# Kernel optimization log

Measured on AMD Instinct MI355X. Metric: run time of the kernel, lower is better.

Reference implementation:

```python
import jax, jax.numpy as jnp
import numpy as np

D_MODEL = 1024
N_HEADS = 16
D_K = D_MODEL // N_HEADS
D_FF = 4096
EPS = 1e-5


def _layernorm(x, g, b):
    mu = jnp.mean(x, axis=-1, keepdims=True)
    var = jnp.mean(jnp.square(x - mu), axis=-1, keepdims=True)
    return (x - mu) * jax.lax.rsqrt(var + EPS) * g + b


def setup_inputs() -> dict:
    key = jax.random.key(0)
    ks = jax.random.split(key, 16)
    s = 0.02
    B, S = 2, 2048
    inp = {
        "x": jax.random.normal(ks[0], (B, S, D_MODEL), dtype=jnp.float32),
        "mask": jnp.ones((1, 1, S, S), dtype=jnp.int32),
        # attention projections (stored [in, out]; y = x @ W + b)
        "Wq": jax.random.normal(ks[1], (D_MODEL, D_MODEL)) * s,
        "bq": jnp.zeros((D_MODEL,)),
        "Wk": jax.random.normal(ks[2], (D_MODEL, D_MODEL)) * s,
        "bk": jnp.zeros((D_MODEL,)),
        "Wv": jax.random.normal(ks[3], (D_MODEL, D_MODEL)) * s,
        "bv": jnp.zeros((D_MODEL,)),
        "Wo": jax.random.normal(ks[4], (D_MODEL, D_MODEL)) * s,
        "bo": jnp.zeros((D_MODEL,)),
        "temperature": jnp.sqrt(jnp.array([float(D_K)], dtype=jnp.float32)),
        "time_weights": jax.random.normal(ks[5], (1, N_HEADS, 1, D_K)),
        "gateW": jax.random.normal(ks[6], (D_K, 1)) * s,
        "gateb": jnp.zeros((1,)),
        "ln_attn_g": jnp.ones((D_MODEL,)),
        "ln_attn_b": jnp.zeros((D_MODEL,)),
        # feed-forward
        "fc1W": jax.random.normal(ks[7], (D_MODEL, D_FF)) * s,
        "fc1b": jnp.zeros((D_FF,)),
        "fc2W": jax.random.normal(ks[8], (D_FF, D_MODEL)) * s,
        "fc2b": jnp.zeros((D_MODEL,)),
        "n1g": jnp.ones((D_MODEL,)),
        "n1b": jnp.zeros((D_MODEL,)),
        "n2g": jnp.ones((D_MODEL,)),
        "n2b": jnp.zeros((D_MODEL,)),
    }
    return inp


def reference(x, mask, Wq, bq, Wk, bk, Wv, bv, Wo, bo, temperature,
              time_weights, gateW, gateb, ln_attn_g, ln_attn_b,
              fc1W, fc1b, fc2W, fc2b, n1g, n1b, n2g, n2b):
    B, S, D = x.shape
    H, dk = N_HEADS, D_K

    def heads(t):  # [B,S,D] -> [B,H,S,dk]
        return t.reshape(B, S, H, dk).transpose(0, 2, 1, 3)

    q = heads(x @ Wq + bq) + time_weights  # learned per-head bias on Q
    k = heads(x @ Wk + bk)
    v = heads(x @ Wv + bv)

    scores = jnp.einsum("bhqd,bhkd->bhqk", q, k) / temperature
    scores = jnp.where(mask == 0, jnp.float32(-1e9), scores)
    gate = jax.nn.sigmoid(q @ gateW + gateb)  # [B,H,S,1] per-query gate
    scores = scores * gate
    probs = jax.nn.softmax(scores, axis=-1)

    ctx = jnp.einsum("bhqk,bhkd->bhqd", probs, v)
    ctx = ctx.transpose(0, 2, 1, 3).reshape(B, S, D)
    attn_out = _layernorm(ctx @ Wo + bo, ln_attn_g, ln_attn_b)

    x1 = _layernorm(x + attn_out, n1g, n1b)
    ff = jax.nn.gelu(x1 @ fc1W + fc1b, approximate=False) @ fc2W + fc2b
    return _layernorm(x1 + ff, n2g, n2b)
```

## Files before the change

### kernel.cpp

```cpp
#include <hip/hip_runtime.h>
#include <stdint.h>
#include <math.h>


typedef uint16_t u16;
typedef unsigned long long u64;
typedef __attribute__((ext_vector_type(8))) short short8;
typedef __attribute__((ext_vector_type(4))) float f32x4;

#define S_LEN 2048
#define DM 1024
#define PSTR 76

#define GLOAD_LDS16(g, l)                                                      \
  __builtin_amdgcn_global_load_lds(                                            \
      (const __attribute__((address_space(1))) void*)(g),                      \
      (__attribute__((address_space(3))) void*)(l), 16, 0, 0)

#define VM0_BARRIER()                                                          \
  do {                                                                         \
    asm volatile("s_waitcnt vmcnt(0)" ::: "memory");                           \
    __builtin_amdgcn_s_barrier();                                              \
  } while (0)

#define LGKM_BARRIER()                                                         \
  do {                                                                         \
    asm volatile("s_waitcnt lgkmcnt(0)" ::: "memory");                         \
    __builtin_amdgcn_s_barrier();                                              \
  } while (0)

__device__ __forceinline__ float bf2f(u16 h) {
  union { uint32_t u; float f; } x;
  x.u = ((uint32_t)h) << 16;
  return x.f;
}
__device__ __forceinline__ u16 f2bf(float f) {
  union { float f; uint32_t u; } x;
  x.f = f;
  uint32_t r = (x.u + 0x7fffu + ((x.u >> 16) & 1u)) >> 16;
  return (u16)r;
}
__device__ __forceinline__ u16 f2bf_fast(float f) {
  union { float f; uint32_t u; } x;
  x.f = f;
  return (u16)((x.u + 0x8000u) >> 16);
}

__device__ __forceinline__ float gelu_ex(float v) {
  float x = fabsf(v) * 0.70710678118654752f;
  float t = __builtin_amdgcn_rcpf(__builtin_fmaf(0.3275911f, x, 1.0f));
  float p = 1.061405429f;
  p = __builtin_fmaf(p, t, -1.453152027f);
  p = __builtin_fmaf(p, t, 1.421413741f);
  p = __builtin_fmaf(p, t, -0.284496736f);
  p = __builtin_fmaf(p, t, 0.254829592f);
  p = p * t;
  float ex = __builtin_amdgcn_exp2f(-1.4426950408889634f * x * x);
  float er = __builtin_fmaf(-p, ex, 1.0f);
  er = (v < 0.f) ? -er : er;
  return 0.5f * v * (1.0f + er);
}

union U8 { uint4 u; u16 s[8]; };
union U4 { uint2 u; u16 s[4]; };

__global__ __launch_bounds__(256) void cvt_k(const float* __restrict__ in,
                                             u16* __restrict__ out, int n) {
  int i = (blockIdx.x * 256 + threadIdx.x) * 4;
  if (i >= n) return;
  float4 v = *(const float4*)(in + i);
  U4 o;
  o.s[0] = f2bf(v.x); o.s[1] = f2bf(v.y); o.s[2] = f2bf(v.z); o.s[3] = f2bf(v.w);
  *(uint2*)(out + i) = o.u;
}

__global__ __launch_bounds__(256) void mb_k(const int* __restrict__ mask,
                                            u16* __restrict__ mb) {
  int tid = blockIdx.x * 256 + threadIdx.x;
  const int* src = mask + (size_t)tid * 16;
  uint32_t b = 0;
#pragma unroll
  for (int q = 0; q < 4; q++) {
    int4 m = *(const int4*)(src + q * 4);
    b |= (m.x != 0 ? 1u : 0u) << (q * 4 + 0);
    b |= (m.y != 0 ? 1u : 0u) << (q * 4 + 1);
    b |= (m.z != 0 ? 1u : 0u) << (q * 4 + 2);
    b |= (m.w != 0 ? 1u : 0u) << (q * 4 + 3);
  }
  mb[tid] = (u16)b;
}

__device__ __forceinline__ void tcvt_body(const float* __restrict__ in,
                                          u16* __restrict__ out, int R, int C) {
  __shared__ u16 tile[64][72];
  int c0 = blockIdx.x * 64, r0 = blockIdx.y * 64;
  int t = threadIdx.x;
  int r = t & 63, seg = t >> 6;
  const float* src = in + (size_t)(r0 + r) * C + c0 + seg * 16;
#pragma unroll
  for (int q = 0; q < 4; q++) {
    float4 v = *(const float4*)(src + q * 4);
    tile[r][seg * 16 + q * 4 + 0] = f2bf(v.x);
    tile[r][seg * 16 + q * 4 + 1] = f2bf(v.y);
    tile[r][seg * 16 + q * 4 + 2] = f2bf(v.z);
    tile[r][seg * 16 + q * 4 + 3] = f2bf(v.w);
  }
  __syncthreads();
  U8 v0, v1;
#pragma unroll
  for (int i = 0; i < 8; i++) v0.s[i] = tile[seg * 16 + i][r];
#pragma unroll
  for (int i = 0; i < 8; i++) v1.s[i] = tile[seg * 16 + 8 + i][r];
  u16* dst = out + (size_t)(c0 + r) * R + r0 + seg * 16;
  *(uint4*)dst = v0.u;
  *(uint4*)(dst + 8) = v1.u;
}

__global__ __launch_bounds__(256) void transpose_cvt_k(const float* __restrict__ in,
                                                       u16* __restrict__ out,
                                                       int R, int C) {
  tcvt_body(in, out, R, C);
}

__global__ __launch_bounds__(256) void transpose_cvt3_k(const float* __restrict__ i0,
                                                        const float* __restrict__ i1,
                                                        const float* __restrict__ i2,
                                                        u16* __restrict__ o0,
                                                        u16* __restrict__ o1,
                                                        u16* __restrict__ o2) {
  int z = blockIdx.z;
  const float* in = (z == 0) ? i0 : (z == 1) ? i1 : i2;
  u16* out = (z == 0) ? o0 : (z == 1) ? o1 : o2;
  tcvt_body(in, out, 1024, 1024);
}

__global__ __launch_bounds__(256) void vtrans_k(const u16* __restrict__ V,
                                                u16* __restrict__ VT) {
  __shared__ u16 tile[64][72];
  int bx = blockIdx.x, bh = blockIdx.y;
  int b = bh >> 4, h = bh & 15;
  int t = threadIdx.x, r = t & 63, seg = t >> 6;
  const u16* src = V + (size_t)(b * S_LEN + bx * 64 + r) * DM + h * 64 + seg * 16;
  *(uint4*)&tile[r][seg * 16] = *(const uint4*)src;
  *(uint4*)&tile[r][seg * 16 + 8] = *(const uint4*)(src + 8);
  __syncthreads();
  U8 v0, v1;
#pragma unroll
  for (int i = 0; i < 8; i++) v0.s[i] = tile[seg * 16 + i][r];
#pragma unroll
  for (int i = 0; i < 8; i++) v1.s[i] = tile[seg * 16 + 8 + i][r];
  u16* dst = VT + ((size_t)bh * 64 + r) * S_LEN + bx * 64 + seg * 16;
  *(uint4*)dst = v0.u;
  *(uint4*)(dst + 8) = v1.u;
}

template <int BM, int EPI, int MXS>
__global__ __launch_bounds__(256) void gemm_bt(const u16* __restrict__ A,
                                               const u16* __restrict__ Bt,
                                               u16* __restrict__ C,
                                               const float* __restrict__ bias,
                                               int M, int N, int K) {
  constexpr int MI = BM / 32;
  constexpr int RPW = BM / 4;
  __shared__ u16 As[2][BM * 32];
  __shared__ u16 Bs[2][128 * 32];
  int t = threadIdx.x;
  int wid = t >> 6, lane = t & 63;
  int g = lane >> 4, li = lane & 15;
  int bx = MXS ? blockIdx.y : blockIdx.x;
  int by = MXS ? blockIdx.x : blockIdx.y;
  int wr = (wid >> 1) * (BM / 2), wc = (wid & 1) * 64;

  const u16* a0 = A + (size_t)(by * BM + wid * RPW + (lane >> 2)) * K + (lane & 3) * 8;
  const u16* b0 = Bt + (size_t)(bx * 128 + wid * 32 + (lane >> 2)) * K + (lane & 3) * 8;
  u16* lA[2] = {&As[0][wid * RPW * 32], &As[1][wid * RPW * 32]};
  u16* lB[2] = {&Bs[0][wid * 1024], &Bs[1][wid * 1024]};

  f32x4 acc[MI][4];
#pragma unroll
  for (int i = 0; i < MI; i++)
#pragma unroll
    for (int j = 0; j < 4; j++) acc[i][j] = (f32x4){0.f, 0.f, 0.f, 0.f};

  auto stage = [&](int buf, int kk) {
    GLOAD_LDS16(a0 + kk, lA[buf]);
    if (BM == 128) GLOAD_LDS16(a0 + (size_t)16 * K + kk, lA[buf] + 512);
    GLOAD_LDS16(b0 + kk, lB[buf]);
    GLOAD_LDS16(b0 + (size_t)16 * K + kk, lB[buf] + 512);
  };
  auto compute = [&](int buf) {
    short8 af[MI], bfv[4];
#pragma unroll
    for (int i = 0; i < MI; i++)
      af[i] = *(const short8*)&As[buf][(wr + i * 16 + li) * 32 + g * 8];
#pragma unroll
    for (int i = 0; i < 4; i++)
      bfv[i] = *(const short8*)&Bs[buf][(wc + i * 16 + li) * 32 + g * 8];
    __builtin_amdgcn_s_setprio(1);
#pragma unroll
    for (int mi = 0; mi < MI; mi++)
#pragma unroll
      for (int ni = 0; ni < 4; ni++)
        acc[mi][ni] = __builtin_amdgcn_mfma_f32_16x16x32_bf16(
            af[mi], bfv[ni], acc[mi][ni], 0, 0, 0);
    __builtin_amdgcn_s_setprio(0);
  };

  stage(0, 0);
  VM0_BARRIER();
  for (int k0 = 0; k0 < K; k0 += 64) {
    stage(1, k0 + 32);
    compute(0);
    VM0_BARRIER();
    if (k0 + 64 < K) stage(0, k0 + 64);
    compute(1);
    VM0_BARRIER();
  }

#pragma unroll
  for (int ni = 0; ni < 4; ni++) {
    int col = bx * 128 + wc + ni * 16 + li;
    float bv = bias[col];
#pragma unroll
    for (int mi = 0; mi < MI; mi++) {
#pragma unroll
      for (int r = 0; r < 4; r++) {
        int row = by * BM + wr + mi * 16 + g * 4 + r;
        float v = acc[mi][ni][r] + bv;
        if (EPI == 2) v = gelu_ex(v);
        C[(size_t)row * N + col] = f2bf(v);
      }
    }
  }
}

__global__ __launch_bounds__(256) void qkv_gemm(const u16* __restrict__ A,
                                                const u16* __restrict__ WTq,
                                                const u16* __restrict__ WTk,
                                                const u16* __restrict__ WTv,
                                                u16* __restrict__ Cq,
                                                u16* __restrict__ Ck,
                                                u16* __restrict__ Cv,
                                                const float* __restrict__ bq,
                                                const float* __restrict__ bk,
                                                const float* __restrict__ bv,
                                                const float* __restrict__ tw) {
  const int K = 1024, N = 1024;
  __shared__ u16 As[2][128 * 32];
  __shared__ u16 Bs[2][128 * 32];
  int t = threadIdx.x;
  int wid = t >> 6, lane = t & 63;
  int g = lane >> 4, li = lane & 15;
  int by = blockIdx.x, bx = blockIdx.y, z = blockIdx.z;
  int wr = (wid >> 1) * 64, wc = (wid & 1) * 64;

  const u16* Bt = (z == 0) ? WTq : (z == 1) ? WTk : WTv;
  u16* C = (z == 0) ? Cq : (z == 1) ? Ck : Cv;
  const float* bias = (z == 0) ? bq : (z == 1) ? bk : bv;

  const u16* a0 = A + (size_t)(by * 128 + wid * 32 + (lane >> 2)) * K + (lane & 3) * 8;
  const u16* b0 = Bt + (size_t)(bx * 128 + wid * 32 + (lane >> 2)) * K + (lane & 3) * 8;
  u16* lA[2] = {&As[0][wid * 1024], &As[1][wid * 1024]};
  u16* lB[2] = {&Bs[0][wid * 1024], &Bs[1][wid * 1024]};

  f32x4 acc[4][4];
#pragma unroll
  for (int i = 0; i < 4; i++)
#pragma unroll
    for (int j = 0; j < 4; j++) acc[i][j] = (f32x4){0.f, 0.f, 0.f, 0.f};

  auto stage = [&](int buf, int kk) {
    GLOAD_LDS16(a0 + kk, lA[buf]);
    GLOAD_LDS16(a0 + (size_t)16 * K + kk, lA[buf] + 512);
    GLOAD_LDS16(b0 + kk, lB[buf]);
    GLOAD_LDS16(b0 + (size_t)16 * K + kk, lB[buf] + 512);
  };
  auto compute = [&](int buf) {
    short8 af[4], bfv[4];
#pragma unroll
    for (int i = 0; i < 4; i++)
      af[i] = *(const short8*)&As[buf][(wr + i * 16 + li) * 32 + g * 8];
#pragma unroll
    for (int i = 0; i < 4; i++)
      bfv[i] = *(const short8*)&Bs[buf][(wc + i * 16 + li) * 32 + g * 8];
    __builtin_amdgcn_s_setprio(1);
#pragma unroll
    for (int mi = 0; mi < 4; mi++)
#pragma unroll
      for (int ni = 0; ni < 4; ni++)
        acc[mi][ni] = __builtin_amdgcn_mfma_f32_16x16x32_bf16(
            af[mi], bfv[ni], acc[mi][ni], 0, 0, 0);
    __builtin_amdgcn_s_setprio(0);
  };

  stage(0, 0);
  VM0_BARRIER();
  for (int k0 = 0; k0 < K; k0 += 64) {
    stage(1, k0 + 32);
    compute(0);
    VM0_BARRIER();
    if (k0 + 64 < K) stage(0, k0 + 64);
    compute(1);
    VM0_BARRIER();
  }

#pragma unroll
  for (int ni = 0; ni < 4; ni++) {
    int col = bx * 128 + wc + ni * 16 + li;
    float bvv = bias[col];
    if (z == 0) bvv += tw[col];
#pragma unroll
    for (int mi = 0; mi < 4; mi++) {
#pragma unroll
      for (int r = 0; r < 4; r++) {
        int row = by * 128 + wr + mi * 16 + g * 4 + r;
        C[(size_t)row * N + col] = f2bf(acc[mi][ni][r] + bvv);
      }
    }
  }
}

__global__ __launch_bounds__(256) void attn_k(const u16* __restrict__ Q,
                                              const u16* __restrict__ Kp,
                                              const u16* __restrict__ VT,
                                              u16* __restrict__ CTX,
                                              const u16* __restrict__ mb,
                                              const float* __restrict__ gateW,
                                              const float* __restrict__ gateb,
                                              const float* __restrict__ temp) {
  __shared__ u16 QPs[64 * PSTR];
  __shared__ u16 Ks[64][72];
  __shared__ u16 Vs[64][72];
  __shared__ float gate_s[64];

  int blk = blockIdx.x;
  int bh = blk & 31, qt = blk >> 5;
  int b = bh >> 4, h = bh & 15;
  int t = threadIdx.x, wid = t >> 6, lane = t & 63;
  int g = lane >> 4, li = lane & 15;
  int sq0 = qt * 64;
  int rr = t >> 2, cc = (t & 3) * 16;

  const u16* Qb  = Q + ((size_t)b * S_LEN) * DM + h * 64;
  const u16* Kb  = Kp + ((size_t)b * S_LEN) * DM + h * 64;
  const u16* VTb = VT + ((size_t)(b * 16 + h) * 64) * S_LEN;

  {
    const u16* src = Qb + (size_t)(sq0 + rr) * DM + cc;
    *(uint4*)&QPs[rr * PSTR + cc] = *(const uint4*)src;
    *(uint4*)&QPs[rr * PSTR + cc + 8] = *(const uint4*)(src + 8);
  }
  __syncthreads();
  {
    U8 q0, q1;
    q0.u = *(const uint4*)&QPs[rr * PSTR + cc];
    q1.u = *(const uint4*)&QPs[rr * PSTR + cc + 8];
    float4 w0 = *(const float4*)(gateW + cc);
    float4 w1 = *(const float4*)(gateW + cc + 4);
    float4 w2 = *(const float4*)(gateW + cc + 8);
    float4 w3 = *(const float4*)(gateW + cc + 12);
    float acc;
    acc  = bf2f(q0.s[0]) * w0.x + bf2f(q0.s[1]) * w0.y +
           bf2f(q0.s[2]) * w0.z + bf2f(q0.s[3]) * w0.w;
    acc += bf2f(q0.s[4]) * w1.x + bf2f(q0.s[5]) * w1.y +
           bf2f(q0.s[6]) * w1.z + bf2f(q0.s[7]) * w1.w;
    acc += bf2f(q1.s[0]) * w2.x + bf2f(q1.s[1]) * w2.y +
           bf2f(q1.s[2]) * w2.z + bf2f(q1.s[3]) * w2.w;
    acc += bf2f(q1.s[4]) * w3.x + bf2f(q1.s[5]) * w3.y +
           bf2f(q1.s[6]) * w3.z + bf2f(q1.s[7]) * w3.w;
    acc += __shfl_xor(acc, 1, 64);
    acc += __shfl_xor(acc, 2, 64);
    if ((t & 3) == 0) gate_s[rr] = 1.f / (1.f + __expf(-(acc + gateb[0])));
  }
  __syncthreads();

  const float LOG2E = 1.4426950408889634f;
  float invt2 = LOG2E / temp[0];
  float cng = -1.0e9f * temp[0];
  short8 qf0 = *(const short8*)&QPs[(wid * 16 + li) * PSTR + g * 8];
  short8 qf1 = *(const short8*)&QPs[(wid * 16 + li) * PSTR + 32 + g * 8];
  float gqs[4];
  int row0 = sq0 + wid * 16 + g * 4;
#pragma unroll
  for (int r = 0; r < 4; r++) gqs[r] = gate_s[wid * 16 + g * 4 + r] * invt2;
  const u16* mbp = mb + (size_t)row0 * 128;

  float m_i[4], psl[4];
  f32x4 o[4];
#pragma unroll
  for (int r = 0; r < 4; r++) { m_i[r] = -1e30f; psl[r] = 0.f; }
#pragma unroll
  for (int n = 0; n < 4; n++) o[n] = (f32x4){0.f, 0.f, 0.f, 0.f};

  uint4 kxa, kxb, vxa, vxb;
  {
    const u16* sK = Kb + (size_t)rr * DM + cc;
    kxa = *(const uint4*)sK; kxb = *(const uint4*)(sK + 8);
    const u16* sV = VTb + (size_t)rr * S_LEN + cc;
    vxa = *(const uint4*)sV; vxb = *(const uint4*)(sV + 8);
  }

  for (int kt = 0; kt < 32; kt++) {
    LGKM_BARRIER();
    *(uint4*)&Ks[rr][cc]     = kxa;
    *(uint4*)&Ks[rr][cc + 8] = kxb;
    *(uint4*)&Vs[rr][cc]     = vxa;
    *(uint4*)&Vs[rr][cc + 8] = vxb;
    u64 bits[4];
#pragma unroll
    for (int r = 0; r < 4; r++)
      bits[r] = *(const u64*)(mbp + (size_t)r * 128 + kt * 4);
    if (kt + 1 < 32) {
      const u16* sK = Kb + (size_t)((kt + 1) * 64 + rr) * DM + cc;
      kxa = *(const uint4*)sK; kxb = *(const uint4*)(sK + 8);
      const u16* sV = VTb + (size_t)rr * S_LEN + (kt + 1) * 64 + cc;
      vxa = *(const uint4*)sV; vxb = *(const uint4*)(sV + 8);
    }
    LGKM_BARRIER();

    f32x4 sc[4];
#pragma unroll
    for (int ni = 0; ni < 4; ni++) {
      sc[ni] = (f32x4){0.f, 0.f, 0.f, 0.f};
      short8 kf0 = *(const short8*)&Ks[ni * 16 + li][g * 8];
      short8 kf1 = *(const short8*)&Ks[ni * 16 + li][32 + g * 8];
      sc[ni] = __builtin_amdgcn_mfma_f32_16x16x32_bf16(qf0, kf0, sc[ni], 0, 0, 0);
      sc[ni] = __builtin_amdgcn_mfma_f32_16x16x32_bf16(qf1, kf1, sc[ni], 0, 0, 0);
    }

    float rmax[4] = {-1e30f, -1e30f, -1e30f, -1e30f};
    bool allm = ((bits[0] & bits[1] & bits[2] & bits[3]) == ~0ull);
    if (__all(allm)) {
#pragma unroll
      for (int ni = 0; ni < 4; ni++)
#pragma unroll
        for (int r = 0; r < 4; r++) {
          float s = sc[ni][r] * gqs[r];
          sc[ni][r] = s;
          rmax[r] = fmaxf(rmax[r], s);
        }
    } else {
      u64 bs[4];
#pragma unroll
      for (int r = 0; r < 4; r++) bs[r] = bits[r] >> li;
#pragma unroll
      for (int ni = 0; ni < 4; ni++)
#pragma unroll
        for (int r = 0; r < 4; r++) {
          float s = ((bs[r] >> (ni * 16)) & 1ull) ? sc[ni][r] * gqs[r]
                                                  : gqs[r] * cng;
          sc[ni][r] = s;
          rmax[r] = fmaxf(rmax[r], s);
        }
    }
#pragma unroll
    for (int off = 1; off < 16; off <<= 1)
#pragma unroll
      for (int r = 0; r < 4; r++)
        rmax[r] = fmaxf(rmax[r], __shfl_xor(rmax[r], off, 64));

    bool need = false;
#pragma unroll
    for (int r = 0; r < 4; r++) need = need || (rmax[r] > m_i[r] + 8.f);
    if (__any(need)) {
#pragma unroll
      for (int r = 0; r < 4; r++) {
        float mnew = fmaxf(m_i[r], rmax[r]);
        float alpha = __builtin_amdgcn_exp2f(m_i[r] - mnew);
        m_i[r] = mnew;
        psl[r] *= alpha;
#pragma unroll
        for (int n = 0; n < 4; n++) o[n][r] *= alpha;
      }
    }

    float pp[4] = {0.f, 0.f, 0.f, 0.f};
#pragma unroll
    for (int ni = 0; ni < 4; ni++)
#pragma unroll
      for (int r = 0; r < 4; r++) {
        float p = __builtin_amdgcn_exp2f(sc[ni][r] - m_i[r]);
        pp[r] += p;
        QPs[(wid * 16 + g * 4 + r) * PSTR + ni * 16 + li] = f2bf_fast(p);
      }
#pragma unroll
    for (int r = 0; r < 4; r++) psl[r] += pp[r];

    __builtin_amdgcn_wave_barrier();

    short8 pf0 = *(const short8*)&QPs[(wid * 16 + li) * PSTR + g * 8];
    short8 pf1 = *(const short8*)&QPs[(wid * 16 + li) * PSTR + 32 + g * 8];
#pragma unroll
    for (int ni = 0; ni < 4; ni++) {
      short8 vf0 = *(const short8*)&Vs[ni * 16 + li][g * 8];
      short8 vf1 = *(const short8*)&Vs[ni * 16 + li][32 + g * 8];
      o[ni] = __builtin_amdgcn_mfma_f32_16x16x32_bf16(pf0, vf0, o[ni], 0, 0, 0);
      o[ni] = __builtin_amdgcn_mfma_f32_16x16x32_bf16(pf1, vf1, o[ni], 0, 0, 0);
    }
  }

  float linv[4];
#pragma unroll
  for (int r = 0; r < 4; r++) {
    float l = psl[r];
#pragma unroll
    for (int off = 1; off < 16; off <<= 1) l += __shfl_xor(l, off, 64);
    linv[r] = 1.f / l;
  }
#pragma unroll
  for (int ni = 0; ni < 4; ni++) {
    int col = h * 64 + ni * 16 + li;
#pragma unroll
    for (int r = 0; r < 4; r++) {
      size_t row = (size_t)b * S_LEN + row0 + r;
      CTX[row * DM + col] = f2bf(o[ni][r] * linv[r]);
    }
  }
}

__device__ __forceinline__ void block_sum2(float& a, float& b, float* red, int t) {
#pragma unroll
  for (int off = 32; off > 0; off >>= 1) {
    a += __shfl_xor(a, off, 64);
    b += __shfl_xor(b, off, 64);
  }
  __syncthreads();
  if ((t & 63) == 0) {
    red[(t >> 6) * 2] = a;
    red[(t >> 6) * 2 + 1] = b;
  }
  __syncthreads();
  a = red[0] + red[2] + red[4] + red[6];
  b = red[1] + red[3] + red[5] + red[7];
}

__global__ __launch_bounds__(256) void ln1_k(const u16* __restrict__ po,
                                             const float* __restrict__ x,
                                             const float* __restrict__ g1,
                                             const float* __restrict__ b1,
                                             const float* __restrict__ g2,
                                             const float* __restrict__ b2,
                                             u16* __restrict__ x1) {
  __shared__ float red[8];
  int row = blockIdx.x, t = threadIdx.x;
  size_t base = (size_t)row * 1024 + t * 4;
  U4 pv; pv.u = *(const uint2*)(po + base);
  float v[4];
#pragma unroll
  for (int i = 0; i < 4; i++) v[i] = bf2f(pv.s[i]);
  float s1 = v[0] + v[1] + v[2] + v[3];
  float s2 = v[0]*v[0] + v[1]*v[1] + v[2]*v[2] + v[3]*v[3];
  block_sum2(s1, s2, red, t);
  float mu = s1 * (1.f / 1024.f);
  float rs = rsqrtf(s2 * (1.f / 1024.f) - mu * mu + 1e-5f);
  float4 xv = *(const float4*)(x + base);
  float4 g1v = *(const float4*)(g1 + t * 4);
  float4 b1v = *(const float4*)(b1 + t * 4);
  float w[4];
  w[0] = xv.x + ((v[0] - mu) * rs * g1v.x + b1v.x);
  w[1] = xv.y + ((v[1] - mu) * rs * g1v.y + b1v.y);
  w[2] = xv.z + ((v[2] - mu) * rs * g1v.z + b1v.z);
  w[3] = xv.w + ((v[3] - mu) * rs * g1v.w + b1v.w);
  s1 = w[0] + w[1] + w[2] + w[3];
  s2 = w[0]*w[0] + w[1]*w[1] + w[2]*w[2] + w[3]*w[3];
  block_sum2(s1, s2, red, t);
  mu = s1 * (1.f / 1024.f);
  rs = rsqrtf(s2 * (1.f / 1024.f) - mu * mu + 1e-5f);
  float4 g2v = *(const float4*)(g2 + t * 4);
  float4 b2v = *(const float4*)(b2 + t * 4);
  U4 ov;
  ov.s[0] = f2bf((w[0] - mu) * rs * g2v.x + b2v.x);
  ov.s[1] = f2bf((w[1] - mu) * rs * g2v.y + b2v.y);
  ov.s[2] = f2bf((w[2] - mu) * rs * g2v.z + b2v.z);
  ov.s[3] = f2bf((w[3] - mu) * rs * g2v.w + b2v.w);
  *(uint2*)(x1 + base) = ov.u;
}

__global__ __launch_bounds__(256) void ln2_k(const u16* __restrict__ y,
                                             const u16* __restrict__ x1,
                                             const float* __restrict__ g,
                                             const float* __restrict__ b,
                                             float* __restrict__ out) {
  __shared__ float red[8];
  int row = blockIdx.x, t = threadIdx.x;
  size_t base = (size_t)row * 1024 + t * 4;
  U4 yv; yv.u = *(const uint2*)(y + base);
  U4 xv; xv.u = *(const uint2*)(x1 + base);
  float w[4];
#pragma unroll
  for (int i = 0; i < 4; i++) w[i] = bf2f(yv.s[i]) + bf2f(xv.s[i]);
  float s1 = w[0] + w[1] + w[2] + w[3];
  float s2 = w[0]*w[0] + w[1]*w[1] + w[2]*w[2] + w[3]*w[3];
  block_sum2(s1, s2, red, t);
  float mu = s1 * (1.f / 1024.f);
  float rs = rsqrtf(s2 * (1.f / 1024.f) - mu * mu + 1e-5f);
  float4 gv = *(const float4*)(g + t * 4);
  float4 bv = *(const float4*)(b + t * 4);
  float4 ov;
  ov.x = (w[0] - mu) * rs * gv.x + bv.x;
  ov.y = (w[1] - mu) * rs * gv.y + bv.y;
  ov.z = (w[2] - mu) * rs * gv.z + bv.z;
  ov.w = (w[3] - mu) * rs * gv.w + bv.w;
  *(float4*)(out + base) = ov;
}

extern "C" void kernel_launch(void* const* d_in, const int* in_sizes, int n_in,
                              void* d_out, int out_size, void* d_ws, size_t ws_size,
                              hipStream_t stream) {
  (void)in_sizes; (void)n_in; (void)out_size;
  const float* x    = (const float*)d_in[0];
  const int*   mask = (const int*)d_in[1];
  const float* Wq = (const float*)d_in[2];  const float* bq = (const float*)d_in[3];
  const float* Wk = (const float*)d_in[4];  const float* bk = (const float*)d_in[5];
  const float* Wv = (const float*)d_in[6];  const float* bv = (const float*)d_in[7];
  const float* Wo = (const float*)d_in[8];  const float* bo = (const float*)d_in[9];
  const float* temp = (const float*)d_in[10];
  const float* tw   = (const float*)d_in[11];
  const float* gW   = (const float*)d_in[12]; const float* gb  = (const float*)d_in[13];
  const float* lag  = (const float*)d_in[14]; const float* lab = (const float*)d_in[15];
  const float* f1W  = (const float*)d_in[16]; const float* f1b = (const float*)d_in[17];
  const float* f2W  = (const float*)d_in[18]; const float* f2b = (const float*)d_in[19];
  const float* n1g  = (const float*)d_in[20]; const float* n1b = (const float*)d_in[21];
  const float* n2g  = (const float*)d_in[22]; const float* n2b = (const float*)d_in[23];
  float* out = (float*)d_out;

  u16* ws = (u16*)d_ws;
  const size_t MB4 = (size_t)4096 * 1024;
  u16* s0 = ws;
  u16* s1 = ws + 1 * MB4;
  u16* s2 = ws + 2 * MB4;
  u16* s3 = ws + 3 * MB4;
  u16* s4 = ws + 4 * MB4;
  u16* d0 = (u16*)d_out;
  u16* d1 = d0 + MB4;
  bool bigws = ws_size >= (size_t)9 * 8 * 1024 * 1024;
  u16* Hfull = ws + 5 * MB4;

  dim3 blk(256);
  cvt_k<<<dim3(4096), blk, 0, stream>>>(x, s4, 4096 * 1024);
  transpose_cvt3_k<<<dim3(16, 16, 3), blk, 0, stream>>>(Wq, Wk, Wv, s0, s1, s2);
  qkv_gemm<<<dim3(32, 8, 3), blk, 0, stream>>>(s4, s0, s1, s2, s3, d0, d1,
                                               bq, bk, bv, tw);
  vtrans_k<<<dim3(32, 32), blk, 0, stream>>>(d1, s0);
  mb_k<<<dim3(1024), blk, 0, stream>>>(mask, s1);
  transpose_cvt_k<<<dim3(16, 16), blk, 0, stream>>>(Wo, s4, 1024, 1024);
  attn_k<<<dim3(1024), blk, 0, stream>>>(s3, d0, s0, s2, s1, gW, gb, temp);
  gemm_bt<64, 0, 1><<<dim3(64, 8), blk, 0, stream>>>(s2, s4, d0, bo, 4096, 1024, 1024);
  ln1_k<<<dim3(4096), blk, 0, stream>>>(d0, x, lag, lab, n1g, n1b, s3);
  transpose_cvt_k<<<dim3(64, 16), blk, 0, stream>>>(f1W, s0, 1024, 4096);
  transpose_cvt_k<<<dim3(16, 64), blk, 0, stream>>>(f2W, s1, 4096, 1024);
  if (bigws) {
    gemm_bt<128, 2, 0><<<dim3(32, 32), blk, 0, stream>>>(s3, s0, Hfull, f1b,
                                                         4096, 4096, 1024);
    gemm_bt<64, 0, 0><<<dim3(8, 64), blk, 0, stream>>>(Hfull, s1, s2, f2b,
                                                       4096, 1024, 4096);
  } else {
    for (int i = 0; i < 2; i++) {
      const u16* Ai = s3 + (size_t)i * 2048 * 1024;
      u16* Yi = s2 + (size_t)i * 2048 * 1024;
      gemm_bt<128, 2, 0><<<dim3(32, 16), blk, 0, stream>>>(Ai, s0, d0, f1b,
                                                           2048, 4096, 1024);
      gemm_bt<64, 0, 1><<<dim3(32, 8), blk, 0, stream>>>(d0, s1, Yi, f2b,
                                                         2048, 1024, 4096);
    }
  }
  ln2_k<<<dim3(4096), blk, 0, stream>>>(s2, s3, n2g, n2b, out);
}
```

Before: 468.0 us.

## Split attention key tiles across two wave groups and merge softmax partials

The attention kernel now launches 512 threads per block. Eight waves split each 64-key tile into two halves, so each wave handles 16 query rows against 32 keys. At the end the two halves' running max, sum and output accumulators are merged through shared memory using rescaling factors. This adds intra-block parallelism and shortens each wave's per-tile critical path, at the cost of a final merge step, extra shared memory and more threads per block.

New measurement: 485.1 us. 3.7% more time.

```diff
diff --git a/kernel.cpp b/kernel.cpp
--- a/kernel.cpp
+++ b/kernel.cpp
@@ -4,6 +4,7 @@
 
 
 typedef uint16_t u16;
+typedef uint32_t u32;
 typedef unsigned long long u64;
 typedef __attribute__((ext_vector_type(8))) short short8;
 typedef __attribute__((ext_vector_type(4))) float f32x4;
@@ -320,7 +321,7 @@
   }
 }
 
-__global__ __launch_bounds__(256) void attn_k(const u16* __restrict__ Q,
+__global__ __launch_bounds__(512) void attn_k(const u16* __restrict__ Q,
                                               const u16* __restrict__ Kp,
                                               const u16* __restrict__ VT,
                                               u16* __restrict__ CTX,
@@ -328,61 +329,54 @@
                                               const float* __restrict__ gateW,
                                               const float* __restrict__ gateb,
                                               const float* __restrict__ temp) {
-  __shared__ u16 QPs[64 * PSTR];
-  __shared__ u16 Ks[64][72];
-  __shared__ u16 Vs[64][72];
+  __shared__ u16 QPs[128 * PSTR];
+  __shared__ u16 KV[2 * 64 * 72];
   __shared__ float gate_s[64];
+  __shared__ float mps[4][16][2];
+
+  u16* Ks = KV;
+  u16* Vs = KV + 64 * 72;
 
   int blk = blockIdx.x;
   int bh = blk & 31, qt = blk >> 5;
   int b = bh >> 4, h = bh & 15;
   int t = threadIdx.x, wid = t >> 6, lane = t & 63;
   int g = lane >> 4, li = lane & 15;
+  int rg = wid & 3, kh = wid >> 2;
   int sq0 = qt * 64;
-  int rr = t >> 2, cc = (t & 3) * 16;
+  int rr = t >> 3, cs = (t & 7) * 8;
 
   const u16* Qb  = Q + ((size_t)b * S_LEN) * DM + h * 64;
   const u16* Kb  = Kp + ((size_t)b * S_LEN) * DM + h * 64;
   const u16* VTb = VT + ((size_t)(b * 16 + h) * 64) * S_LEN;
 
   {
-    const u16* src = Qb + (size_t)(sq0 + rr) * DM + cc;
-    *(uint4*)&QPs[rr * PSTR + cc] = *(const uint4*)src;
-    *(uint4*)&QPs[rr * PSTR + cc + 8] = *(const uint4*)(src + 8);
+    const u16* src = Qb + (size_t)(sq0 + rr) * DM + cs;
+    *(uint4*)&QPs[rr * PSTR + cs] = *(const uint4*)src;
   }
   __syncthreads();
   {
-    U8 q0, q1;
-    q0.u = *(const uint4*)&QPs[rr * PSTR + cc];
-    q1.u = *(const uint4*)&QPs[rr * PSTR + cc + 8];
-    float4 w0 = *(const float4*)(gateW + cc);
-    float4 w1 = *(const float4*)(gateW + cc + 4);
-    float4 w2 = *(const float4*)(gateW + cc + 8);
-    float4 w3 = *(const float4*)(gateW + cc + 12);
-    float acc;
-    acc  = bf2f(q0.s[0]) * w0.x + bf2f(q0.s[1]) * w0.y +
-           bf2f(q0.s[2]) * w0.z + bf2f(q0.s[3]) * w0.w;
-    acc += bf2f(q0.s[4]) * w1.x + bf2f(q0.s[5]) * w1.y +
-           bf2f(q0.s[6]) * w1.z + bf2f(q0.s[7]) * w1.w;
-    acc += bf2f(q1.s[0]) * w2.x + bf2f(q1.s[1]) * w2.y +
-           bf2f(q1.s[2]) * w2.z + bf2f(q1.s[3]) * w2.w;
-    acc += bf2f(q1.s[4]) * w3.x + bf2f(q1.s[5]) * w3.y +
-           bf2f(q1.s[6]) * w3.z + bf2f(q1.s[7]) * w3.w;
+    U8 q0;
+    q0.u = *(const uint4*)&QPs[rr * PSTR + cs];
+    float acc = 0.f;
+#pragma unroll
+    for (int i = 0; i < 8; i++) acc += bf2f(q0.s[i]) * gateW[cs + i];
     acc += __shfl_xor(acc, 1, 64);
     acc += __shfl_xor(acc, 2, 64);
-    if ((t & 3) == 0) gate_s[rr] = 1.f / (1.f + __expf(-(acc + gateb[0])));
+    acc += __shfl_xor(acc, 4, 64);
+    if ((t & 7) == 0) gate_s[rr] = 1.f / (1.f + __expf(-(acc + gateb[0])));
   }
   __syncthreads();
 
   const float LOG2E = 1.4426950408889634f;
   float invt2 = LOG2E / temp[0];
   float cng = -1.0e9f * temp[0];
-  short8 qf0 = *(const short8*)&QPs[(wid * 16 + li) * PSTR + g * 8];
-  short8 qf1 = *(const short8*)&QPs[(wid * 16 + li) * PSTR + 32 + g * 8];
+  short8 qf0 = *(const short8*)&QPs[(rg * 16 + li) * PSTR + g * 8];
+  short8 qf1 = *(const short8*)&QPs[(rg * 16 + li) * PSTR + 32 + g * 8];
   float gqs[4];
-  int row0 = sq0 + wid * 16 + g * 4;
-#pragma unroll
-  for (int r = 0; r < 4; r++) gqs[r] = gate_s[wid * 16 + g * 4 + r] * invt2;
+  int row0 = sq0 + rg * 16 + g * 4;
+#pragma unroll
+  for (int r = 0; r < 4; r++) gqs[r] = gate_s[rg * 16 + g * 4 + r] * invt2;
   const u16* mbp = mb + (size_t)row0 * 128;
 
   float m_i[4], psl[4];
@@ -392,47 +386,42 @@
 #pragma unroll
   for (int n = 0; n < 4; n++) o[n] = (f32x4){0.f, 0.f, 0.f, 0.f};
 
-  uint4 kxa, kxb, vxa, vxb;
+  uint4 kx, vx;
   {
-    const u16* sK = Kb + (size_t)rr * DM + cc;
-    kxa = *(const uint4*)sK; kxb = *(const uint4*)(sK + 8);
-    const u16* sV = VTb + (size_t)rr * S_LEN + cc;
-    vxa = *(const uint4*)sV; vxb = *(const uint4*)(sV + 8);
+    kx = *(const uint4*)(Kb + (size_t)rr * DM + cs);
+    vx = *(const uint4*)(VTb + (size_t)rr * S_LEN + cs);
   }
 
   for (int kt = 0; kt < 32; kt++) {
     LGKM_BARRIER();
-    *(uint4*)&Ks[rr][cc]     = kxa;
-    *(uint4*)&Ks[rr][cc + 8] = kxb;
-    *(uint4*)&Vs[rr][cc]     = vxa;
-    *(uint4*)&Vs[rr][cc + 8] = vxb;
-    u64 bits[4];
+    *(uint4*)&Ks[rr * 72 + cs] = kx;
+    *(uint4*)&Vs[rr * 72 + cs] = vx;
+    u32 bits[4];
 #pragma unroll
     for (int r = 0; r < 4; r++)
-      bits[r] = *(const u64*)(mbp + (size_t)r * 128 + kt * 4);
+      bits[r] = *(const u32*)(mbp + (size_t)r * 128 + kt * 4 + kh * 2);
     if (kt + 1 < 32) {
-      const u16* sK = Kb + (size_t)((kt + 1) * 64 + rr) * DM + cc;
-      kxa = *(const uint4*)sK; kxb = *(const uint4*)(sK + 8);
-      const u16* sV = VTb + (size_t)rr * S_LEN + (kt + 1) * 64 + cc;
-      vxa = *(const uint4*)sV; vxb = *(const uint4*)(sV + 8);
+      kx = *(const uint4*)(Kb + (size_t)((kt + 1) * 64 + rr) * DM + cs);
+      vx = *(const uint4*)(VTb + (size_t)rr * S_LEN + (kt + 1) * 64 + cs);
     }
     LGKM_BARRIER();
 
-    f32x4 sc[4];
-#pragma unroll
-    for (int ni = 0; ni < 4; ni++) {
+    f32x4 sc[2];
+#pragma unroll
+    for (int ni = 0; ni < 2; ni++) {
       sc[ni] = (f32x4){0.f, 0.f, 0.f, 0.f};
-      short8 kf0 = *(const short8*)&Ks[ni * 16 + li][g * 8];
-      short8 kf1 = *(const short8*)&Ks[ni * 16 + li][32 + g * 8];
+      const u16* kr = &Ks[(kh * 32 + ni * 16 + li) * 72];
+      short8 kf0 = *(const short8*)(kr + g * 8);
+      short8 kf1 = *(const short8*)(kr + 32 + g * 8);
       sc[ni] = __builtin_amdgcn_mfma_f32_16x16x32_bf16(qf0, kf0, sc[ni], 0, 0, 0);
       sc[ni] = __builtin_amdgcn_mfma_f32_16x16x32_bf16(qf1, kf1, sc[ni], 0, 0, 0);
     }
 
     float rmax[4] = {-1e30f, -1e30f, -1e30f, -1e30f};
-    bool allm = ((bits[0] & bits[1] & bits[2] & bits[3]) == ~0ull);
+    bool allm = ((bits[0] & bits[1] & bits[2] & bits[3]) == 0xFFFFFFFFu);
     if (__all(allm)) {
 #pragma unroll
-      for (int ni = 0; ni < 4; ni++)
+      for (int ni = 0; ni < 2; ni++)
 #pragma unroll
         for (int r = 0; r < 4; r++) {
           float s = sc[ni][r] * gqs[r];
@@ -440,15 +429,15 @@
           rmax[r] = fmaxf(rmax[r], s);
         }
     } else {
-      u64 bs[4];
+      u32 bs[4];
 #pragma unroll
       for (int r = 0; r < 4; r++) bs[r] = bits[r] >> li;
 #pragma unroll
-      for (int ni = 0; ni < 4; ni++)
+      for (int ni = 0; ni < 2; ni++)
 #pragma unroll
         for (int r = 0; r < 4; r++) {
-          float s = ((bs[r] >> (ni * 16)) & 1ull) ? sc[ni][r] * gqs[r]
-                                                  : gqs[r] * cng;
+          float s = ((bs[r] >> (ni * 16)) & 1u) ? sc[ni][r] * gqs[r]
+                                                : gqs[r] * cng;
           sc[ni][r] = s;
           rmax[r] = fmaxf(rmax[r], s);
         }
@@ -476,7 +465,7 @@
 
     float pp[4] = {0.f, 0.f, 0.f, 0.f};
 #pragma unroll
-    for (int ni = 0; ni < 4; ni++)
+    for (int ni = 0; ni < 2; ni++)
 #pragma unroll
       for (int r = 0; r < 4; r++) {
         float p = __builtin_amdgcn_exp2f(sc[ni][r] - m_i[r]);
@@ -488,32 +477,60 @@
 
     __builtin_amdgcn_wave_barrier();
 
-    short8 pf0 = *(const short8*)&QPs[(wid * 16 + li) * PSTR + g * 8];
-    short8 pf1 = *(const short8*)&QPs[(wid * 16 + li) * PSTR + 32 + g * 8];
+    short8 pf = *(const short8*)&QPs[(wid * 16 + li) * PSTR + g * 8];
 #pragma unroll
     for (int ni = 0; ni < 4; ni++) {
-      short8 vf0 = *(const short8*)&Vs[ni * 16 + li][g * 8];
-      short8 vf1 = *(const short8*)&Vs[ni * 16 + li][32 + g * 8];
-      o[ni] = __builtin_amdgcn_mfma_f32_16x16x32_bf16(pf0, vf0, o[ni], 0, 0, 0);
-      o[ni] = __builtin_amdgcn_mfma_f32_16x16x32_bf16(pf1, vf1, o[ni], 0, 0, 0);
-    }
-  }
-
-  float linv[4];
+      short8 vf = *(const short8*)&Vs[(ni * 16 + li) * 72 + kh * 32 + g * 8];
+      o[ni] = __builtin_amdgcn_mfma_f32_16x16x32_bf16(pf, vf, o[ni], 0, 0, 0);
+    }
+  }
+
 #pragma unroll
   for (int r = 0; r < 4; r++) {
     float l = psl[r];
 #pragma unroll
     for (int off = 1; off < 16; off <<= 1) l += __shfl_xor(l, off, 64);
-    linv[r] = 1.f / l;
-  }
-#pragma unroll
-  for (int ni = 0; ni < 4; ni++) {
-    int col = h * 64 + ni * 16 + li;
+    psl[r] = l;
+  }
+
+  __syncthreads();
+  float* Oscr = (float*)KV;
+  if (kh == 1) {
+#pragma unroll
+    for (int ni = 0; ni < 4; ni++)
+#pragma unroll
+      for (int r = 0; r < 4; r++)
+        Oscr[rg * 1024 + (g * 4 + r) * 64 + ni * 16 + li] = o[ni][r];
+    if (li == 0) {
+#pragma unroll
+      for (int r = 0; r < 4; r++) {
+        mps[rg][g * 4 + r][0] = m_i[r];
+        mps[rg][g * 4 + r][1] = psl[r];
+      }
+    }
+  }
+  __syncthreads();
+  if (kh == 0) {
+    float sa[4], sb[4], linv[4];
 #pragma unroll
     for (int r = 0; r < 4; r++) {
-      size_t row = (size_t)b * S_LEN + row0 + r;
-      CTX[row * DM + col] = f2bf(o[ni][r] * linv[r]);
+      float mB = mps[rg][g * 4 + r][0];
+      float lB = mps[rg][g * 4 + r][1];
+      float mT = fmaxf(m_i[r], mB);
+      sa[r] = __builtin_amdgcn_exp2f(m_i[r] - mT);
+      sb[r] = __builtin_amdgcn_exp2f(mB - mT);
+      linv[r] = 1.f / (psl[r] * sa[r] + lB * sb[r]);
+    }
+#pragma unroll
+    for (int ni = 0; ni < 4; ni++) {
+      int col = h * 64 + ni * 16 + li;
+#pragma unroll
+      for (int r = 0; r < 4; r++) {
+        float ob = Oscr[rg * 1024 + (g * 4 + r) * 64 + ni * 16 + li];
+        size_t row = (size_t)b * S_LEN + row0 + r;
+        CTX[row * DM + col] =
+            f2bf((o[ni][r] * sa[r] + ob * sb[r]) * linv[r]);
+      }
     }
   }
 }
@@ -644,7 +661,7 @@
   vtrans_k<<<dim3(32, 32), blk, 0, stream>>>(d1, s0);
   mb_k<<<dim3(1024), blk, 0, stream>>>(mask, s1);
   transpose_cvt_k<<<dim3(16, 16), blk, 0, stream>>>(Wo, s4, 1024, 1024);
-  attn_k<<<dim3(1024), blk, 0, stream>>>(s3, d0, s0, s2, s1, gW, gb, temp);
+  attn_k<<<dim3(1024), dim3(512), 0, stream>>>(s3, d0, s0, s2, s1, gW, gb, temp);
   gemm_bt<64, 0, 1><<<dim3(64, 8), blk, 0, stream>>>(s2, s4, d0, bo, 4096, 1024, 1024);
   ln1_k<<<dim3(4096), blk, 0, stream>>>(d0, x, lag, lab, n1g, n1b, s3);
   transpose_cvt_k<<<dim3(64, 16), blk, 0, stream>>>(f1W, s0, 1024, 4096);
```
